# Kernel optimization log

Measured on AMD Instinct MI355X. Metric: run time of the kernel, lower is better.

Reference implementation:

```python
import jax, jax.numpy as jnp
import numpy as np

D_MODEL = 512
NUM_HEADS = 8
DEPTH = D_MODEL // NUM_HEADS
PROJ_DIM = 256
SEQ_LEN = 4096
BATCH = 8


def _glorot(key, shape):
    fan_in, fan_out = shape[-2], shape[-1]
    limit = np.sqrt(6.0 / (fan_in + fan_out))
    return jax.random.uniform(key, shape, jnp.float32, -limit, limit)


def setup_inputs() -> dict:
    key = jax.random.key(0)
    ks = jax.random.split(key, 8)
    x = jax.random.normal(ks[0], (BATCH, SEQ_LEN, D_MODEL), jnp.float32)
    wq = _glorot(ks[1], (D_MODEL, D_MODEL))
    wk = _glorot(ks[2], (D_MODEL, D_MODEL))
    wv = _glorot(ks[3], (D_MODEL, D_MODEL))
    E = _glorot(ks[4], (NUM_HEADS, SEQ_LEN, PROJ_DIM))
    F = _glorot(ks[5], (NUM_HEADS, SEQ_LEN, PROJ_DIM))
    w_out = _glorot(ks[6], (D_MODEL, D_MODEL))
    b_out = jnp.zeros((D_MODEL,), jnp.float32)
    return {"x": x, "wq": wq, "wk": wk, "wv": wv, "E": E, "F": F,
            "w_out": w_out, "b_out": b_out}


def reference(x, wq, wk, wv, E, F, w_out, b_out):
    b, n, _ = x.shape
    # QKV projections + split heads -> [b, h, n, d]
    def split_heads(t):
        return t.reshape(b, n, NUM_HEADS, DEPTH).transpose(0, 2, 1, 3)
    q = split_heads(x @ wq)
    k = split_heads(x @ wk)
    v = split_heads(x @ wv)
    # Linformer low-rank projection of K/V along sequence: [b,h,r,d]
    k_proj = jnp.einsum('bhnd,hnr->bhrd', k, E)
    v_proj = jnp.einsum('bhnd,hnr->bhrd', v, F)
    scale = 1.0 / jnp.sqrt(jnp.asarray(DEPTH, jnp.float32))
    scores = jnp.einsum('bhnd,bhrd->bhnr', q, k_proj) * scale  # [b,h,n,r]
    attn = jax.nn.softmax(scores, axis=-1)
    out = jnp.einsum('bhnr,bhrd->bhnd', attn, v_proj)
    out = out.transpose(0, 2, 1, 3).reshape(b, n, D_MODEL)
    return out @ w_out + b_out
```

## Files before the change

kernel.cpp:

```cpp
#include <hip/hip_runtime.h>

typedef unsigned short u16;
typedef unsigned int   u32;
typedef __bf16 bf16x8 __attribute__((ext_vector_type(8)));
typedef float  f32x4  __attribute__((ext_vector_type(4)));
typedef u16    u16x4  __attribute__((ext_vector_type(4)));

#define DEV __device__ __forceinline__

DEV u16 f2bf(float f) {
    u32 u = __builtin_bit_cast(u32, f);
    u = (u + 0x7fffu + ((u >> 16) & 1u)) >> 16;
    return (u16)u;
}

DEV void gload16(const void* g, void* l) {
    __builtin_amdgcn_global_load_lds((const __attribute__((address_space(1))) u32*)g,
                                     (__attribute__((address_space(3))) u32*)l, 16, 0, 0);
}

DEV void vmw(int n) {
    switch (n) {
        case 0:  asm volatile("s_waitcnt vmcnt(0)" ::: "memory"); break;
        case 4:  asm volatile("s_waitcnt vmcnt(4)" ::: "memory"); break;
        default: asm volatile("s_waitcnt vmcnt(8)" ::: "memory"); break;
    }
}

__global__ __launch_bounds__(256) void k_prep(const float* __restrict__ x,
                                              const float* __restrict__ wq, const float* __restrict__ wk,
                                              const float* __restrict__ wv, const float* __restrict__ wo,
                                              const float* __restrict__ E, const float* __restrict__ F,
                                              u16* __restrict__ xb, u16* __restrict__ wcatT, u16* __restrict__ woT,
                                              u16* __restrict__ Et, u16* __restrict__ Ft) {
    __shared__ u16 tile[64][68];
    const int t = threadIdx.x;
    const int bid = blockIdx.x;
    if (bid < 16384) {
        int i = (bid * 256 + t) * 4;
        float4 v = *(const float4*)(x + i);
        u16x4 o;
        o[0] = f2bf(v.x); o[1] = f2bf(v.y); o[2] = f2bf(v.z); o[3] = f2bf(v.w);
        *(u16x4*)(xb + i) = o;
    } else if (bid < 20480) {
        const int b2 = bid - 16384;
        const int rt = b2 & 3, ntl = (b2 >> 2) & 63, h = (b2 >> 8) & 7, which = b2 >> 11;
        const float* src = (which ? F : E) + (size_t)h * 4096 * 256;
        u16* dst = (which ? Ft : Et) + (size_t)h * 256 * 4096;
        const int n0 = ntl * 64, r0 = rt * 64;
#pragma unroll
        for (int it = 0; it < 4; ++it) {
            const int idx = t + it * 256;
            const int nl = idx >> 4, rq = (idx & 15) * 4;
            float4 v = *(const float4*)(src + (size_t)(n0 + nl) * 256 + r0 + rq);
            tile[rq + 0][nl] = f2bf(v.x);
            tile[rq + 1][nl] = f2bf(v.y);
            tile[rq + 2][nl] = f2bf(v.z);
            tile[rq + 3][nl] = f2bf(v.w);
        }
        __syncthreads();
#pragma unroll
        for (int it = 0; it < 4; ++it) {
            const int idx = t + it * 256;
            const int rl = idx >> 4, nq = (idx & 15) * 4;
            u16x4 vv = *(const u16x4*)&tile[rl][nq];
            *(u16x4*)(dst + (size_t)(r0 + rl) * 4096 + n0 + nq) = vv;
        }
    } else {
        const int b2 = bid - 20480;
        const int mi = b2 >> 6, tix = b2 & 63;
        const int jt = tix & 7, kt = tix >> 3;
        const float* w = (mi == 0) ? wq : (mi == 1) ? wk : (mi == 2) ? wv : wo;
        u16* dst = (mi < 3) ? (wcatT + mi * 262144) : woT;
#pragma unroll
        for (int it = 0; it < 4; ++it) {
            const int idx = t + it * 256;
            const int kl = idx >> 4, jq = (idx & 15) * 4;
            float4 v = *(const float4*)(w + (size_t)(kt * 64 + kl) * 512 + jt * 64 + jq);
            tile[jq + 0][kl] = f2bf(v.x);
            tile[jq + 1][kl] = f2bf(v.y);
            tile[jq + 2][kl] = f2bf(v.z);
            tile[jq + 3][kl] = f2bf(v.w);
        }
        __syncthreads();
#pragma unroll
        for (int it = 0; it < 4; ++it) {
            const int idx = t + it * 256;
            const int jl = idx >> 4, kq = (idx & 15) * 4;
            u16x4 vv = *(const u16x4*)&tile[jl][kq];
            *(u16x4*)(dst + (size_t)(jt * 64 + jl) * 512 + kt * 64 + kq) = vv;
        }
    }
}

template <int MODE>
__global__ __launch_bounds__(512, 2) void k_gemm8(const u16* __restrict__ A, const u16* __restrict__ Bm,
                                                  u16* __restrict__ Qo, u16* __restrict__ Kt, u16* __restrict__ Vt,
                                                  float* __restrict__ Of, const float* __restrict__ bias,
                                                  int M, int N, int K) {
    __shared__ __attribute__((aligned(16))) char smem[131072];
    const int tid = threadIdx.x;
    const int lane = tid & 63, w = tid >> 6;
    const int wr = w >> 2, wcn = w & 3;
    const int g = lane >> 4, l16 = lane & 15;
    const int nbm = M >> 8;
    const int bnc = N >> 8;
    const int bandw = nbm >> 3;
    const int bid = (int)blockIdx.x;
    const int xcd = bid & 7, loc = bid >> 3;
    const int bm = xcd * bandw + loc / bnc;
    const int bn = loc % bnc;
    const int m0 = bm << 8, n0 = bn << 8;
    const int NP = K >> 5;

    auto stage_pair = [&](int P) {
        const int kt = P >> 1, kh = P & 1;
        const int slot = P & 3;
#pragma unroll
        for (int isB = 0; isB < 2; ++isB) {
            const u16* src = isB ? Bm : A;
            const int r0 = isB ? n0 : m0;
            char* base = smem + isB * 65536 + slot * 16384;
#pragma unroll
            for (int j = 0; j < 2; ++j) {
                const int off = j * 8192 + tid * 16;
                const int row = off >> 6, c = (off >> 4) & 3;
                const int sc = c ^ ((row >> 1) & 3);
                gload16(src + (size_t)(r0 + row) * K + kt * 64 + kh * 32 + sc * 8, base + off);
            }
        }
    };

    stage_pair(0); stage_pair(1); stage_pair(2);
    vmw(8);
    __builtin_amdgcn_sched_barrier(0);
    __builtin_amdgcn_s_barrier();

    f32x4 acc[8][4] = {};
    for (int P = 0; P < NP; ++P) {
        const int slot = P & 3;
        char* abase = smem + slot * 16384;
        char* bbase = smem + 65536 + slot * 16384;
        bf16x8 av[8], bv[4];
#pragma unroll
        for (int m = 0; m < 8; ++m) {
            const int row = wr * 128 + m * 16 + l16;
            const int c = g ^ ((row >> 1) & 3);
            av[m] = *(const bf16x8*)(abase + row * 64 + c * 16);
        }
#pragma unroll
        for (int n = 0; n < 4; ++n) {
            const int col = wcn * 64 + n * 16 + l16;
            const int c = g ^ ((col >> 1) & 3);
            bv[n] = *(const bf16x8*)(bbase + col * 64 + c * 16);
        }
        if (P + 3 < NP) stage_pair(P + 3);
        __builtin_amdgcn_s_setprio(1);
#pragma unroll
        for (int m = 0; m < 8; ++m)
#pragma unroll
            for (int n = 0; n < 4; ++n)
                acc[m][n] = __builtin_amdgcn_mfma_f32_16x16x32_bf16(av[m], bv[n], acc[m][n], 0, 0, 0);
        __builtin_amdgcn_s_setprio(0);
        if (P < NP - 1) {
            vmw(P < NP - 3 ? 8 : (P == NP - 3 ? 4 : 0));
            __builtin_amdgcn_sched_barrier(0);
            __builtin_amdgcn_s_barrier();
        }
    }

    if (MODE == 0) {
        if (n0 < 512) {
#pragma unroll
            for (int m = 0; m < 8; ++m)
#pragma unroll
                for (int jn = 0; jn < 4; ++jn) {
                    const int col = n0 + wcn * 64 + jn * 16 + l16;
#pragma unroll
                    for (int i = 0; i < 4; ++i) {
                        const int row = m0 + wr * 128 + m * 16 + g * 4 + i;
                        Qo[(size_t)row * 512 + col] = f2bf(acc[m][jn][i]);
                    }
                }
        } else {
            u16* dst = (n0 < 1024) ? Kt : Vt;
#pragma unroll
            for (int m = 0; m < 8; ++m)
#pragma unroll
                for (int jn = 0; jn < 4; ++jn) {
                    const int col = (n0 + wcn * 64 + jn * 16 + l16) & 511;
                    const int h = col >> 6, d = col & 63;
                    const int rowb = m0 + wr * 128 + m * 16 + g * 4;
                    const int b = rowb >> 12, nn = rowb & 4095;
                    u16x4 pk;
#pragma unroll
                    for (int i = 0; i < 4; ++i) pk[i] = f2bf(acc[m][jn][i]);
                    *(u16x4*)(dst + ((size_t)((b * 8 + h) * 64 + d)) * 4096 + nn) = pk;
                }
        }
    } else {
#pragma unroll
        for (int m = 0; m < 8; ++m)
#pragma unroll
            for (int jn = 0; jn < 4; ++jn) {
                const int col = n0 + wcn * 64 + jn * 16 + l16;
                const float bb = bias[col];
#pragma unroll
                for (int i = 0; i < 4; ++i) {
                    const int row = m0 + wr * 128 + m * 16 + g * 4 + i;
                    Of[(size_t)row * N + col] = acc[m][jn][i] + bb;
                }
            }
    }
}

__global__ __launch_bounds__(256) void k_proj(const u16* __restrict__ Et, const u16* __restrict__ Ft,
                                              const u16* __restrict__ Kt, const u16* __restrict__ Vt,
                                              float* __restrict__ pbuf) {
    __shared__ __attribute__((aligned(16))) char smem[24576];
    const int tid = threadIdx.x;
    const int lane = tid & 63, wid = tid >> 6;
    const int wr = wid >> 1, wc = wid & 1;
    const int g = lane >> 4, l16 = lane & 15;
    const int bid = blockIdx.x;
    const int sp = bid >> 8, rest = bid & 255;
    const int mt = rest & 1, which = (rest >> 1) & 1, bh = rest >> 2;
    const int h = bh & 7;
    const u16* Ap = (which ? Ft : Et) + (size_t)h * 256 * 4096 + (size_t)mt * 128 * 4096;
    const u16* Bp = (which ? Vt : Kt) + (size_t)bh * 64 * 4096;

    f32x4 acc[4][2] = {};

    const int kbeg = sp * 1024;
    for (int k0 = kbeg; k0 < kbeg + 1024; k0 += 64) {
#pragma unroll
        for (int c = 0; c < 4; ++c) {
            const int off = c * 4096 + tid * 16;
            const int row = off >> 7;
            const int sc = ((off >> 4) & 7) ^ (row & 7);
            gload16(Ap + (size_t)row * 4096 + (k0 + sc * 8), smem + off);
            if (c < 2)
                gload16(Bp + (size_t)row * 4096 + (k0 + sc * 8), smem + 16384 + off);
        }
        __syncthreads();
#pragma unroll
        for (int kk = 0; kk < 64; kk += 32) {
            bf16x8 av[4], bv[2];
#pragma unroll
            for (int m = 0; m < 4; ++m) {
                const int r = wr * 64 + m * 16 + l16;
                av[m] = *(const bf16x8*)(smem + r * 128 + ((kk * 2 + g * 16) ^ ((r & 7) << 4)));
            }
#pragma unroll
            for (int n = 0; n < 2; ++n) {
                const int r = wc * 32 + n * 16 + l16;
                bv[n] = *(const bf16x8*)(smem + 16384 + r * 128 + ((kk * 2 + g * 16) ^ ((r & 7) << 4)));
            }
            __builtin_amdgcn_s_setprio(1);
#pragma unroll
            for (int m = 0; m < 4; ++m)
#pragma unroll
                for (int n = 0; n < 2; ++n)
                    acc[m][n] = __builtin_amdgcn_mfma_f32_16x16x32_bf16(av[m], bv[n], acc[m][n], 0, 0, 0);
            __builtin_amdgcn_s_setprio(0);
        }
        __syncthreads();
    }

    float* pb = pbuf + ((size_t)(sp * 2 + which) * 64 + bh) * 16384;
    if (which == 0) {
#pragma unroll
        for (int m = 0; m < 4; ++m)
#pragma unroll
            for (int n = 0; n < 2; ++n) {
                const int d = wc * 32 + n * 16 + l16;
#pragma unroll
                for (int i = 0; i < 4; ++i) {
                    const int rg = mt * 128 + wr * 64 + m * 16 + g * 4 + i;
                    pb[rg * 64 + d] = acc[m][n][i];
                }
            }
    } else {
#pragma unroll
        for (int m = 0; m < 4; ++m)
#pragma unroll
            for (int n = 0; n < 2; ++n) {
                const int d = wc * 32 + n * 16 + l16;
                const int r4 = mt * 128 + wr * 64 + m * 16 + g * 4;
                *(f32x4*)(pb + d * 256 + r4) = acc[m][n];
            }
    }
}

__global__ __launch_bounds__(256) void k_preduce(const float* __restrict__ pbuf, u16* __restrict__ outkv) {
    const int o = ((int)blockIdx.x * 256 + (int)threadIdx.x) * 4;
    f32x4 s = *(const f32x4*)(pbuf + o);
    s += *(const f32x4*)(pbuf + 2097152 + o);
    s += *(const f32x4*)(pbuf + 4194304 + o);
    s += *(const f32x4*)(pbuf + 6291456 + o);
    u16x4 r;
#pragma unroll
    for (int i = 0; i < 4; ++i) r[i] = f2bf(s[i]);
    *(u16x4*)(outkv + o) = r;
}

__global__ __launch_bounds__(512) void k_flash(const u16* __restrict__ Q, const u16* __restrict__ kp,
                                               const u16* __restrict__ vpT, u16* __restrict__ ctx) {
    __shared__ __attribute__((aligned(16))) char smem[131072];
    const int tid = threadIdx.x;
    const int lane = tid & 63, w = tid >> 6;
    const int g = lane >> 4, l16 = lane & 15;
    const int bid = blockIdx.x;
    const int seg = bid & 7, bh = bid >> 3;
    const int b = bh >> 3, h = bh & 7;
    const int n0 = seg * 512;

#pragma unroll
    for (int c = 0; c < 4; ++c) {
        const int off = c * 8192 + tid * 16;
        {
            const int row = off >> 7;
            const int sc = ((off >> 4) & 7) ^ (row & 7);
            gload16(kp + (size_t)bh * 16384 + row * 64 + sc * 8, smem + off);
        }
        {
            const int row = off >> 9;
            const int sc = ((off >> 4) & 31) ^ (row & 7);
            gload16(vpT + (size_t)bh * 16384 + row * 256 + sc * 8, smem + 32768 + off);
        }
    }
    const size_t qrow0 = (size_t)(b * 4096 + n0 + w * 16 + l16) * 512 + h * 64 + g * 8;
    bf16x8 qf0 = *(const bf16x8*)(Q + qrow0);
    bf16x8 qf1 = *(const bf16x8*)(Q + qrow0 + 32);
    __syncthreads();

    const int pbase = 65536 + w * 8192;
    for (int qp = 0; qp < 4; ++qp) {
        f32x4 s[16];
        __builtin_amdgcn_s_setprio(1);
#pragma unroll
        for (int rt = 0; rt < 16; ++rt) {
            const int r = rt * 16 + l16;
            const int sw = (r & 7) << 4;
            bf16x8 kv0 = *(const bf16x8*)(smem + r * 128 + ((g * 16) ^ sw));
            bf16x8 kv1 = *(const bf16x8*)(smem + r * 128 + ((64 + g * 16) ^ sw));
            f32x4 z = {0.f, 0.f, 0.f, 0.f};
            z = __builtin_amdgcn_mfma_f32_16x16x32_bf16(qf0, kv0, z, 0, 0, 0);
            z = __builtin_amdgcn_mfma_f32_16x16x32_bf16(qf1, kv1, z, 0, 0, 0);
            s[rt] = z;
        }
        __builtin_amdgcn_s_setprio(0);

        if (qp < 3) {
            const size_t qn = qrow0 + (size_t)(qp + 1) * 128 * 512;
            qf0 = *(const bf16x8*)(Q + qn);
            qf1 = *(const bf16x8*)(Q + qn + 32);
        }

        float mx[4] = {-1e30f, -1e30f, -1e30f, -1e30f};
#pragma unroll
        for (int rt = 0; rt < 16; ++rt)
#pragma unroll
            for (int i = 0; i < 4; ++i) {
                s[rt][i] *= 0.125f;
                mx[i] = fmaxf(mx[i], s[rt][i]);
            }
#pragma unroll
        for (int i = 0; i < 4; ++i) {
            mx[i] = fmaxf(mx[i], __shfl_xor(mx[i], 1));
            mx[i] = fmaxf(mx[i], __shfl_xor(mx[i], 2));
            mx[i] = fmaxf(mx[i], __shfl_xor(mx[i], 4));
            mx[i] = fmaxf(mx[i], __shfl_xor(mx[i], 8));
        }
        float sm[4] = {0.f, 0.f, 0.f, 0.f};
#pragma unroll
        for (int rt = 0; rt < 16; ++rt)
#pragma unroll
            for (int i = 0; i < 4; ++i) {
                float e = __expf(s[rt][i] - mx[i]);
                s[rt][i] = e;
                sm[i] += e;
            }
#pragma unroll
        for (int i = 0; i < 4; ++i) {
            sm[i] += __shfl_xor(sm[i], 1);
            sm[i] += __shfl_xor(sm[i], 2);
            sm[i] += __shfl_xor(sm[i], 4);
            sm[i] += __shfl_xor(sm[i], 8);
        }

#pragma unroll
        for (int rt = 0; rt < 16; ++rt)
#pragma unroll
            for (int i = 0; i < 4; ++i) {
                const int nrow = g * 4 + i;
                const int byte = pbase + nrow * 512 + ((rt * 32 + l16 * 2) ^ ((nrow & 7) << 4));
                *(u16*)(smem + byte) = f2bf(s[rt][i]);
            }
        bf16x8 af[8];
#pragma unroll
        for (int ks = 0; ks < 8; ++ks) {
            const int byte = pbase + l16 * 512 + ((ks * 64 + g * 16) ^ ((l16 & 7) << 4));
            af[ks] = *(const bf16x8*)(smem + byte);
        }
        f32x4 o[4] = {};
        __builtin_amdgcn_s_setprio(1);
#pragma unroll
        for (int dt = 0; dt < 4; ++dt)
#pragma unroll
            for (int ks = 0; ks < 8; ++ks) {
                const int row = dt * 16 + l16;
                const int byte = 32768 + row * 512 + ((ks * 64 + g * 16) ^ ((row & 7) << 4));
                bf16x8 bv = *(const bf16x8*)(smem + byte);
                o[dt] = __builtin_amdgcn_mfma_f32_16x16x32_bf16(af[ks], bv, o[dt], 0, 0, 0);
            }
        __builtin_amdgcn_s_setprio(0);
        float rinv[4];
#pragma unroll
        for (int i = 0; i < 4; ++i) rinv[i] = 1.0f / sm[i];
#pragma unroll
        for (int dt = 0; dt < 4; ++dt)
#pragma unroll
            for (int i = 0; i < 4; ++i) {
                const int row = b * 4096 + n0 + qp * 128 + w * 16 + g * 4 + i;
                const int col = h * 64 + dt * 16 + l16;
                ctx[(size_t)row * 512 + col] = f2bf(o[dt][i] * rinv[i]);
            }
    }
}


extern "C" void kernel_launch(void* const* d_in, const int* in_sizes, int n_in,
                              void* d_out, int out_size, void* d_ws, size_t ws_size,
                              hipStream_t stream) {
    const float* x  = (const float*)d_in[0];
    const float* wq = (const float*)d_in[1];
    const float* wk = (const float*)d_in[2];
    const float* wv = (const float*)d_in[3];
    const float* E  = (const float*)d_in[4];
    const float* F  = (const float*)d_in[5];
    const float* wo = (const float*)d_in[6];
    const float* bo = (const float*)d_in[7];
    float* out = (float*)d_out;
    u16* ws = (u16*)d_ws;

    u16* xb    = ws;
    u16* Qm    = ws + 16777216;
    u16* Kt    = ws + 33554432;
    u16* Vt    = ws + 50331648;
    u16* Et    = ws + 67108864;
    u16* Ft    = ws + 75497472;
    u16* wcatT = ws + 83886080;
    u16* woT   = ws + 84672512;
    u16* kpB   = ws + 84934656;
    u16* vpT   = ws + 85983232;
    float* pbuf = (float*)xb;
    u16* ctx   = xb;

    k_prep<<<20736, 256, 0, stream>>>(x, wq, wk, wv, wo, E, F, xb, wcatT, woT, Et, Ft);
    k_gemm8<0><<<768, 512, 0, stream>>>(xb, wcatT, Qm, Kt, Vt, nullptr, nullptr, 32768, 1536, 512);
    k_proj<<<1024, 256, 0, stream>>>(Et, Ft, Kt, Vt, pbuf);
    k_preduce<<<2048, 256, 0, stream>>>(pbuf, kpB);
    k_flash<<<512, 512, 0, stream>>>(Qm, kpB, vpT, ctx);
    k_gemm8<1><<<256, 512, 0, stream>>>(ctx, woT, nullptr, nullptr, nullptr, out, bo, 32768, 512, 512);
}
```

Measured before the change: 375.6 us.

## Replace 4-slot LDS pipeline with double buffering in bf16 GEMM

The GEMM kernel shrinks its shared-memory pipeline from four staged K-slices (128 KB) to a two-slot double buffer (64 KB). Each iteration now waits for all outstanding loads before the barrier, and launch bounds are raised to request more resident workgroups per CU. This trades prefetch depth, and so memory-latency hiding, for lower LDS use and potentially higher occupancy. The kernel is renamed and both launches are updated.

```diff
diff --git a/kernel.cpp b/kernel.cpp
--- a/kernel.cpp
+++ b/kernel.cpp
@@ -17,14 +17,6 @@
 DEV void gload16(const void* g, void* l) {
     __builtin_amdgcn_global_load_lds((const __attribute__((address_space(1))) u32*)g,
                                      (__attribute__((address_space(3))) u32*)l, 16, 0, 0);
-}
-
-DEV void vmw(int n) {
-    switch (n) {
-        case 0:  asm volatile("s_waitcnt vmcnt(0)" ::: "memory"); break;
-        case 4:  asm volatile("s_waitcnt vmcnt(4)" ::: "memory"); break;
-        default: asm volatile("s_waitcnt vmcnt(8)" ::: "memory"); break;
-    }
 }
 
 __global__ __launch_bounds__(256) void k_prep(const float* __restrict__ x,
@@ -94,11 +86,11 @@
 }
 
 template <int MODE>
-__global__ __launch_bounds__(512, 2) void k_gemm8(const u16* __restrict__ A, const u16* __restrict__ Bm,
+__global__ __launch_bounds__(512, 4) void k_gemm2(const u16* __restrict__ A, const u16* __restrict__ Bm,
                                                   u16* __restrict__ Qo, u16* __restrict__ Kt, u16* __restrict__ Vt,
                                                   float* __restrict__ Of, const float* __restrict__ bias,
                                                   int M, int N, int K) {
-    __shared__ __attribute__((aligned(16))) char smem[131072];
+    __shared__ __attribute__((aligned(16))) char smem[65536];
     const int tid = threadIdx.x;
     const int lane = tid & 63, w = tid >> 6;
     const int wr = w >> 2, wcn = w & 3;
@@ -113,34 +105,32 @@
     const int m0 = bm << 8, n0 = bn << 8;
     const int NP = K >> 5;
 
-    auto stage_pair = [&](int P) {
-        const int kt = P >> 1, kh = P & 1;
-        const int slot = P & 3;
+    auto stage = [&](int P) {
+        const int slot = P & 1;
 #pragma unroll
         for (int isB = 0; isB < 2; ++isB) {
             const u16* src = isB ? Bm : A;
             const int r0 = isB ? n0 : m0;
-            char* base = smem + isB * 65536 + slot * 16384;
+            char* base = smem + slot * 32768 + isB * 16384;
 #pragma unroll
             for (int j = 0; j < 2; ++j) {
                 const int off = j * 8192 + tid * 16;
                 const int row = off >> 6, c = (off >> 4) & 3;
                 const int sc = c ^ ((row >> 1) & 3);
-                gload16(src + (size_t)(r0 + row) * K + kt * 64 + kh * 32 + sc * 8, base + off);
+                gload16(src + (size_t)(r0 + row) * K + P * 32 + sc * 8, base + off);
             }
         }
     };
 
-    stage_pair(0); stage_pair(1); stage_pair(2);
-    vmw(8);
+    stage(0);
+    asm volatile("s_waitcnt vmcnt(0)" ::: "memory");
     __builtin_amdgcn_sched_barrier(0);
     __builtin_amdgcn_s_barrier();
 
     f32x4 acc[8][4] = {};
     for (int P = 0; P < NP; ++P) {
-        const int slot = P & 3;
-        char* abase = smem + slot * 16384;
-        char* bbase = smem + 65536 + slot * 16384;
+        char* abase = smem + (P & 1) * 32768;
+        char* bbase = abase + 16384;
         bf16x8 av[8], bv[4];
 #pragma unroll
         for (int m = 0; m < 8; ++m) {
@@ -154,7 +144,7 @@
             const int c = g ^ ((col >> 1) & 3);
             bv[n] = *(const bf16x8*)(bbase + col * 64 + c * 16);
         }
-        if (P + 3 < NP) stage_pair(P + 3);
+        if (P + 1 < NP) stage(P + 1);
         __builtin_amdgcn_s_setprio(1);
 #pragma unroll
         for (int m = 0; m < 8; ++m)
@@ -162,8 +152,8 @@
             for (int n = 0; n < 4; ++n)
                 acc[m][n] = __builtin_amdgcn_mfma_f32_16x16x32_bf16(av[m], bv[n], acc[m][n], 0, 0, 0);
         __builtin_amdgcn_s_setprio(0);
-        if (P < NP - 1) {
-            vmw(P < NP - 3 ? 8 : (P == NP - 3 ? 4 : 0));
+        if (P + 1 < NP) {
+            asm volatile("s_waitcnt vmcnt(0)" ::: "memory");
             __builtin_amdgcn_sched_barrier(0);
             __builtin_amdgcn_s_barrier();
         }
@@ -458,9 +448,9 @@
     u16* ctx   = xb;
 
     k_prep<<<20736, 256, 0, stream>>>(x, wq, wk, wv, wo, E, F, xb, wcatT, woT, Et, Ft);
-    k_gemm8<0><<<768, 512, 0, stream>>>(xb, wcatT, Qm, Kt, Vt, nullptr, nullptr, 32768, 1536, 512);
+    k_gemm2<0><<<768, 512, 0, stream>>>(xb, wcatT, Qm, Kt, Vt, nullptr, nullptr, 32768, 1536, 512);
     k_proj<<<1024, 256, 0, stream>>>(Et, Ft, Kt, Vt, pbuf);
     k_preduce<<<2048, 256, 0, stream>>>(pbuf, kpB);
     k_flash<<<512, 512, 0, stream>>>(Qm, kpB, vpT, ctx);
-    k_gemm8<1><<<256, 512, 0, stream>>>(ctx, woT, nullptr, nullptr, nullptr, out, bo, 32768, 512, 512);
-}
+    k_gemm2<1><<<256, 512, 0, stream>>>(ctx, woT, nullptr, nullptr, nullptr, out, bo, 32768, 512, 512);
+}
```

Result: slower. 1.191 ms (+217.2%).
